# Performance work log

Measured on AMD Instinct MI355X. Metric: run time of the kernel, lower is better.

Reference implementation:

```python
import jax, jax.numpy as jnp
import numpy as np

M, K, N = 131072, 1024, 512


def setup_inputs() -> dict:
    key = jax.random.key(0)
    k1, k2, k3, k4, k5 = jax.random.split(key, 5)
    scale = 0.02
    return {
        "x": jax.random.normal(k1, (M, K), dtype=jnp.float32),
        "w0": jax.random.uniform(k2, (K,), dtype=jnp.float32, minval=0.9, maxval=1.1),
        "w1": jax.random.normal(k3, (K, N), dtype=jnp.float32) * scale,
        "w2": jax.random.normal(k4, (K, N), dtype=jnp.float32) * scale,
        "w3": jax.random.normal(k5, (N, K), dtype=jnp.float32) * scale,
    }


def reference(x, w0, w1, w2, w3):
    # RMSNorm (no eps, matching the kernel): l = rsqrt(mean(x^2))
    l = jax.lax.rsqrt(jnp.sum(x * x, axis=-1) / K)          # [M]
    x1 = x * l[:, None] * w0[None, :]                        # [M, K]
    x2 = x1 @ w1                                             # gate   [M, N]
    y2 = x1 @ w2                                             # up     [M, N]
    x3 = jax.nn.silu(x2) * y2                                # SiLU-gate [M, N]
    out = x3 @ w3                                            # down   [M, K] (skip_connection=False)
    return out
```

## Files before the change

kernel.cpp:

```cpp
#include <hip/hip_runtime.h>
#include <cstdint>

typedef __attribute__((ext_vector_type(4))) float f32x4;
typedef __attribute__((ext_vector_type(8))) short bf16x8;
typedef __attribute__((ext_vector_type(4))) short bf16x4;

#define DEV static __device__ __forceinline__

DEV unsigned short f2bf(float f) {
    union { float f; unsigned int u; } v; v.f = f;
    unsigned int u = v.u;
    return (unsigned short)((u + 0x7FFFu + ((u >> 16) & 1u)) >> 16);
}

DEV void async_cp16(const void* g, void* l) {
    __builtin_amdgcn_global_load_lds(
        (const __attribute__((address_space(1))) unsigned int*)g,
        (__attribute__((address_space(3))) unsigned int*)l,
        16, 0, 0);
}

DEV void stage_half(const unsigned short* __restrict__ g, long kofs,
                    unsigned short* l, int tid, int gpitch) {
#pragma unroll
    for (int i = 0; i < 2; ++i) {
        int c = i * 512 + tid;
        int row = c >> 3;
        int ss = (c & 7) ^ (row & 7);
        async_cp16(g + (long)row * gpitch + kofs + ss * 8,
                   l + (i * 512 + (tid & 448)) * 8);
    }
}

template <int NT>
DEV void gemm256(const unsigned short* __restrict__ gA,
                 const unsigned short* __restrict__ gB,
                 const int gpitch, unsigned short* lds,
                 f32x4 (&acc)[8][4], const int tid) {
    const int lane = tid & 63;
    const int wv = tid >> 6;
    const int wr = wv >> 2;
    const int wcq = wv & 3;
    const int lhi = lane >> 4, llo = lane & 15;
    const int hb = wcq >> 1;
    const int br0 = (wcq & 1) * 64;

#define MFMA8(AF, BF, RI0, CJ0)                                               \
    _Pragma("unroll") for (int kq = 0; kq < 2; ++kq)                          \
    _Pragma("unroll") for (int i = 0; i < 4; ++i)                             \
    _Pragma("unroll") for (int j = 0; j < 2; ++j)                             \
        acc[RI0 + i][CJ0 + j] = __builtin_amdgcn_mfma_f32_16x16x32_bf16(      \
            AF[kq][i], BF[kq][j], acc[RI0 + i][CJ0 + j], 0, 0, 0);

    stage_half(gA, 0, lds + 0 * 8192, tid, gpitch);
    stage_half(gA + (long)128 * gpitch, 0, lds + 1 * 8192, tid, gpitch);
    stage_half(gB, 0, lds + 32768 + 0 * 8192, tid, gpitch);
    stage_half(gB + (long)128 * gpitch, 0, lds + 32768 + 1 * 8192, tid, gpitch);
    if (NT > 1) {
        stage_half(gA, 64, lds + 2 * 8192, tid, gpitch);
        asm volatile("s_waitcnt vmcnt(2)" ::: "memory");
    } else {
        asm volatile("s_waitcnt vmcnt(0)" ::: "memory");
    }
    __builtin_amdgcn_s_barrier();

    bf16x8 af[2][4], bf0[2][2], bf1[2][2];

    for (int kt = 0; kt < NT; ++kt) {
        const int cur = kt & 1, nxt = cur ^ 1;
        const unsigned short* lA = lds + (cur * 2 + wr) * 8192;
        const unsigned short* lB = lds + 32768 + (cur * 2 + hb) * 8192;
        const bool pf1 = (kt + 1 < NT);
        const bool pf2 = (kt + 2 < NT);
        const long k1 = (long)(kt + 1) * 64;
        const long k2 = (long)(kt + 2) * 64;

#pragma unroll
        for (int kq = 0; kq < 2; ++kq) {
            const int q = kq * 4 + lhi;
#pragma unroll
            for (int i = 0; i < 4; ++i) {
                int r = i * 16 + llo;
                af[kq][i] = *(const bf16x8*)&lA[r * 64 + ((q ^ (r & 7)) << 3)];
            }
#pragma unroll
            for (int j = 0; j < 2; ++j) {
                int r = br0 + j * 16 + llo;
                bf0[kq][j] = *(const bf16x8*)&lB[r * 64 + ((q ^ (r & 7)) << 3)];
            }
        }
        if (pf1)
            stage_half(gA + (long)128 * gpitch, k1, lds + (nxt * 2 + 1) * 8192, tid, gpitch);
        __builtin_amdgcn_s_barrier();
        asm volatile("s_waitcnt lgkmcnt(0)");
        __builtin_amdgcn_sched_barrier(0);
        __builtin_amdgcn_s_setprio(1);
        MFMA8(af, bf0, 0, 0)
        __builtin_amdgcn_s_setprio(0);
        __builtin_amdgcn_s_barrier();

#pragma unroll
        for (int kq = 0; kq < 2; ++kq) {
            const int q = kq * 4 + lhi;
#pragma unroll
            for (int j = 0; j < 2; ++j) {
                int r = br0 + 32 + j * 16 + llo;
                bf1[kq][j] = *(const bf16x8*)&lB[r * 64 + ((q ^ (r & 7)) << 3)];
            }
        }
        if (pf1) {
            stage_half(gB, k1, lds + 32768 + (nxt * 2 + 0) * 8192, tid, gpitch);
            stage_half(gB + (long)128 * gpitch, k1, lds + 32768 + (nxt * 2 + 1) * 8192, tid, gpitch);
        }
        __builtin_amdgcn_s_barrier();
        asm volatile("s_waitcnt lgkmcnt(0)");
        __builtin_amdgcn_sched_barrier(0);
        __builtin_amdgcn_s_setprio(1);
        MFMA8(af, bf1, 0, 2)
        __builtin_amdgcn_s_setprio(0);
        __builtin_amdgcn_s_barrier();

#pragma unroll
        for (int kq = 0; kq < 2; ++kq) {
            const int q = kq * 4 + lhi;
#pragma unroll
            for (int i = 0; i < 4; ++i) {
                int r = 64 + i * 16 + llo;
                af[kq][i] = *(const bf16x8*)&lA[r * 64 + ((q ^ (r & 7)) << 3)];
            }
        }
        __builtin_amdgcn_s_barrier();
        asm volatile("s_waitcnt lgkmcnt(0)");
        __builtin_amdgcn_sched_barrier(0);
        __builtin_amdgcn_s_setprio(1);
        MFMA8(af, bf0, 4, 0)
        __builtin_amdgcn_s_setprio(0);
        __builtin_amdgcn_s_barrier();

        if (pf2)
            stage_half(gA, k2, lds + (cur * 2 + 0) * 8192, tid, gpitch);
        __builtin_amdgcn_s_setprio(1);
        MFMA8(af, bf1, 4, 2)
        __builtin_amdgcn_s_setprio(0);
        if (pf1) {
            if (pf2) asm volatile("s_waitcnt vmcnt(2)" ::: "memory");
            else     asm volatile("s_waitcnt vmcnt(0)" ::: "memory");
        }
        __builtin_amdgcn_s_barrier();
        __builtin_amdgcn_sched_barrier(0);
    }
#undef MFMA8
}

__global__ void prep_w(const float* __restrict__ w0, const float* __restrict__ w1,
                       const float* __restrict__ w2, const float* __restrict__ w3,
                       unsigned short* __restrict__ w12t, unsigned short* __restrict__ w3t) {
    int t = blockIdx.x * 256 + threadIdx.x;
    if (t < 1048576) {
        int n = t >> 10, k = t & 1023;
        const float* src = (n & 1) ? w2 : w1;
        w12t[t] = f2bf(w0[k] * src[k * 512 + (n >> 1)]);
    } else {
        int idx = t - 1048576;
        int j = idx >> 9, n = idx & 511;
        w3t[idx] = f2bf(w3[n * 1024 + j]);
    }
}

__global__ __launch_bounds__(256)
void prep_x(const float* __restrict__ x, unsigned short* __restrict__ xb) {
    const int wv = threadIdx.x >> 6, lane = threadIdx.x & 63;
    const int stride = gridDim.x * 4;
    for (int row = blockIdx.x * 4 + wv; row < 131072; row += stride) {
        const float* xr = x + (long)row * 1024;
        f32x4 v[4];
        float s = 0.f;
#pragma unroll
        for (int c = 0; c < 4; ++c) {
            v[c] = *(const f32x4*)(xr + c * 256 + lane * 4);
            s += v[c].x * v[c].x + v[c].y * v[c].y + v[c].z * v[c].z + v[c].w * v[c].w;
        }
#pragma unroll
        for (int off = 32; off > 0; off >>= 1) s += __shfl_xor(s, off, 64);
        float l = rsqrtf(s * (1.0f / 1024.0f));
        unsigned short* xo = xb + (long)row * 1024;
#pragma unroll
        for (int c = 0; c < 4; ++c) {
            bf16x4 b;
            b.x = (short)f2bf(v[c].x * l);
            b.y = (short)f2bf(v[c].y * l);
            b.z = (short)f2bf(v[c].z * l);
            b.w = (short)f2bf(v[c].w * l);
            *(bf16x4*)(xo + c * 256 + lane * 4) = b;
        }
    }
}

__global__ __launch_bounds__(512, 2)
void gate_gemm(const unsigned short* __restrict__ xb,
               const unsigned short* __restrict__ w12t,
               unsigned short* __restrict__ x3) {
    __shared__ unsigned short lds[65536];
    const int tid = threadIdx.x;
    const int lane = tid & 63;
    const int wv = tid >> 6;
    const int wr = wv >> 2, wcq = wv & 3;
    const int lhi = lane >> 4, llo = lane & 15;

    int bid = blockIdx.x;
    int wgid = (bid & 7) * 256 + (bid >> 3);
    const int mt = wgid >> 2, nt = wgid & 3;

    f32x4 acc[8][4];
#pragma unroll
    for (int i = 0; i < 8; ++i)
#pragma unroll
        for (int j = 0; j < 4; ++j) acc[i][j] = (f32x4){0.f, 0.f, 0.f, 0.f};

    gemm256<16>(xb + (long)mt * 256 * 1024, w12t + (long)nt * 256 * 1024,
                1024, lds, acc, tid);

#pragma unroll
    for (int ri = 0; ri < 8; ++ri)
#pragma unroll
        for (int rr = 0; rr < 4; ++rr) {
            int R = wr * 128 + ri * 16 + lhi * 4 + rr;
#pragma unroll
            for (int cj = 0; cj < 4; ++cj) {
                float v = acc[ri][cj][rr];
                float p = __shfl_xor(v, 1, 64);
                float g = (lane & 1) ? p : v;
                float u = (lane & 1) ? v : p;
                float s = (g / (1.0f + __expf(-g))) * u;
                if (!(lane & 1))
                    lds[R * 136 + wcq * 32 + cj * 8 + (llo >> 1)] = f2bf(s);
            }
        }
    __syncthreads();
    unsigned short* xg = x3 + (long)(mt * 256) * 512 + nt * 128;
#pragma unroll
    for (int i = 0; i < 8; ++i) {
        int c = i * 512 + tid;
        int row = c >> 4, ch = c & 15;
        *(bf16x8*)(xg + (long)row * 512 + ch * 8) = *(const bf16x8*)&lds[row * 136 + ch * 8];
    }
}

__global__ __launch_bounds__(512, 2)
void down_gemm(const unsigned short* __restrict__ x3,
               const unsigned short* __restrict__ w3t,
               float* __restrict__ out) {
    __shared__ unsigned short lds[65536];
    const int tid = threadIdx.x;
    const int lane = tid & 63;
    const int wv = tid >> 6;
    const int wr = wv >> 2, wcq = wv & 3;
    const int lhi = lane >> 4, llo = lane & 15;

    int bid = blockIdx.x;
    int wgid = (bid & 7) * 256 + (bid >> 3);
    const int mt = wgid >> 2, nt = wgid & 3;

    f32x4 acc[8][4];
#pragma unroll
    for (int i = 0; i < 8; ++i)
#pragma unroll
        for (int j = 0; j < 4; ++j) acc[i][j] = (f32x4){0.f, 0.f, 0.f, 0.f};

    gemm256<8>(x3 + (long)mt * 256 * 512, w3t + (long)nt * 256 * 512,
               512, lds, acc, tid);

    float* op = out + (long)(mt * 256) * 1024 + nt * 256;
#pragma unroll
    for (int ri = 0; ri < 8; ++ri)
#pragma unroll
        for (int rr = 0; rr < 4; ++rr) {
            int R = wr * 128 + ri * 16 + lhi * 4 + rr;
#pragma unroll
            for (int cj = 0; cj < 4; ++cj)
                op[(long)R * 1024 + wcq * 64 + cj * 16 + llo] = acc[ri][cj][rr];
        }
}

extern "C" void kernel_launch(void* const* d_in, const int* in_sizes, int n_in,
                              void* d_out, int out_size, void* d_ws, size_t ws_size,
                              hipStream_t stream) {
    const float* x  = (const float*)d_in[0];
    const float* w0 = (const float*)d_in[1];
    const float* w1 = (const float*)d_in[2];
    const float* w2 = (const float*)d_in[3];
    const float* w3 = (const float*)d_in[4];
    float* out = (float*)d_out;

    unsigned short* w12t = (unsigned short*)d_ws;
    unsigned short* w3t  = w12t + 1024 * 1024;
    unsigned short* x3   = w3t + 1024 * 512;
    unsigned short* xb   = x3 + (size_t)131072 * 512;

    prep_w<<<dim3(6144), dim3(256), 0, stream>>>(w0, w1, w2, w3, w12t, w3t);
    prep_x<<<dim3(2048), dim3(256), 0, stream>>>(x, xb);
    gate_gemm<<<dim3(2048), dim3(512), 0, stream>>>(xb, w12t, x3);
    down_gemm<<<dim3(2048), dim3(512), 0, stream>>>(x3, w3t, out);
}
```

Baseline: 704.9 us.

## Restructure GEMM main loop to one barrier per K-step with LDS-read prefetch

Rewrites the per-K-tile schedule of the 256x256 bf16 MFMA GEMM. The old loop used several workgroup barriers per tile with lgkmcnt waits before each MFMA group. The new loop drops to a single barrier per K-step and relies on compiler-inserted LDS waits. It also prefetches the next tile's first A/B fragments from LDS during the last MFMA group, using an extra af1 register array. This aims to cut barrier stalls and overlap LDS reads with MFMAs, at the cost of higher register pressure and a stricter vmcnt(0) wait, which may expose global-load latency.

```diff
diff --git a/kernel.cpp b/kernel.cpp
--- a/kernel.cpp
+++ b/kernel.cpp
@@ -30,6 +30,10 @@
         async_cp16(g + (long)row * gpitch + kofs + ss * 8,
                    l + (i * 512 + (tid & 448)) * 8);
     }
+}
+
+DEV bf16x8 ldsrd(const unsigned short* base, int r, int q) {
+    return *(const bf16x8*)&base[r * 64 + ((q ^ (r & 7)) << 3)];
 }
 
 template <int NT>
@@ -45,12 +49,11 @@
     const int hb = wcq >> 1;
     const int br0 = (wcq & 1) * 64;
 
-#define MFMA8(AF, BF, RI0, CJ0)                                               \
-    _Pragma("unroll") for (int kq = 0; kq < 2; ++kq)                          \
+#define MG(AF, BF, KQ, RI0, CJ0)                                              \
     _Pragma("unroll") for (int i = 0; i < 4; ++i)                             \
     _Pragma("unroll") for (int j = 0; j < 2; ++j)                             \
         acc[RI0 + i][CJ0 + j] = __builtin_amdgcn_mfma_f32_16x16x32_bf16(      \
-            AF[kq][i], BF[kq][j], acc[RI0 + i][CJ0 + j], 0, 0, 0);
+            AF[KQ][i], BF[KQ][j], acc[RI0 + i][CJ0 + j], 0, 0, 0);
 
     stage_half(gA, 0, lds + 0 * 8192, tid, gpitch);
     stage_half(gA + (long)128 * gpitch, 0, lds + 1 * 8192, tid, gpitch);
@@ -63,93 +66,80 @@
         asm volatile("s_waitcnt vmcnt(0)" ::: "memory");
     }
     __builtin_amdgcn_s_barrier();
-
-    bf16x8 af[2][4], bf0[2][2], bf1[2][2];
+    __builtin_amdgcn_sched_barrier(0);
+
+    bf16x8 af0[2][4], af1[2][4], bf0[2][2], bf1[2][2];
+
+    {
+        const unsigned short* lA = lds + wr * 8192;
+        const unsigned short* lB = lds + 32768 + hb * 8192;
+#pragma unroll
+        for (int i = 0; i < 4; ++i) af0[0][i] = ldsrd(lA, i * 16 + llo, lhi);
+#pragma unroll
+        for (int j = 0; j < 2; ++j) bf0[0][j] = ldsrd(lB, br0 + j * 16 + llo, lhi);
+    }
 
     for (int kt = 0; kt < NT; ++kt) {
         const int cur = kt & 1, nxt = cur ^ 1;
-        const unsigned short* lA = lds + (cur * 2 + wr) * 8192;
-        const unsigned short* lB = lds + 32768 + (cur * 2 + hb) * 8192;
+        const unsigned short* lA  = lds + (cur * 2 + wr) * 8192;
+        const unsigned short* lB  = lds + 32768 + (cur * 2 + hb) * 8192;
+        const unsigned short* lAn = lds + (nxt * 2 + wr) * 8192;
+        const unsigned short* lBn = lds + 32768 + (nxt * 2 + hb) * 8192;
         const bool pf1 = (kt + 1 < NT);
         const bool pf2 = (kt + 2 < NT);
         const long k1 = (long)(kt + 1) * 64;
         const long k2 = (long)(kt + 2) * 64;
 
 #pragma unroll
-        for (int kq = 0; kq < 2; ++kq) {
-            const int q = kq * 4 + lhi;
-#pragma unroll
-            for (int i = 0; i < 4; ++i) {
-                int r = i * 16 + llo;
-                af[kq][i] = *(const bf16x8*)&lA[r * 64 + ((q ^ (r & 7)) << 3)];
-            }
-#pragma unroll
-            for (int j = 0; j < 2; ++j) {
-                int r = br0 + j * 16 + llo;
-                bf0[kq][j] = *(const bf16x8*)&lB[r * 64 + ((q ^ (r & 7)) << 3)];
-            }
-        }
-        if (pf1)
+        for (int i = 0; i < 4; ++i) af0[1][i] = ldsrd(lA, i * 16 + llo, 4 + lhi);
+#pragma unroll
+        for (int j = 0; j < 2; ++j) bf0[1][j] = ldsrd(lB, br0 + j * 16 + llo, 4 + lhi);
+#pragma unroll
+        for (int kq = 0; kq < 2; ++kq)
+#pragma unroll
+            for (int j = 0; j < 2; ++j)
+                bf1[kq][j] = ldsrd(lB, br0 + 32 + j * 16 + llo, kq * 4 + lhi);
+        if (pf1) {
             stage_half(gA + (long)128 * gpitch, k1, lds + (nxt * 2 + 1) * 8192, tid, gpitch);
-        __builtin_amdgcn_s_barrier();
-        asm volatile("s_waitcnt lgkmcnt(0)");
-        __builtin_amdgcn_sched_barrier(0);
-        __builtin_amdgcn_s_setprio(1);
-        MFMA8(af, bf0, 0, 0)
-        __builtin_amdgcn_s_setprio(0);
-        __builtin_amdgcn_s_barrier();
-
-#pragma unroll
-        for (int kq = 0; kq < 2; ++kq) {
-            const int q = kq * 4 + lhi;
-#pragma unroll
-            for (int j = 0; j < 2; ++j) {
-                int r = br0 + 32 + j * 16 + llo;
-                bf1[kq][j] = *(const bf16x8*)&lB[r * 64 + ((q ^ (r & 7)) << 3)];
-            }
-        }
-        if (pf1) {
             stage_half(gB, k1, lds + 32768 + (nxt * 2 + 0) * 8192, tid, gpitch);
             stage_half(gB + (long)128 * gpitch, k1, lds + 32768 + (nxt * 2 + 1) * 8192, tid, gpitch);
         }
-        __builtin_amdgcn_s_barrier();
-        asm volatile("s_waitcnt lgkmcnt(0)");
-        __builtin_amdgcn_sched_barrier(0);
-        __builtin_amdgcn_s_setprio(1);
-        MFMA8(af, bf1, 0, 2)
-        __builtin_amdgcn_s_setprio(0);
-        __builtin_amdgcn_s_barrier();
-
-#pragma unroll
-        for (int kq = 0; kq < 2; ++kq) {
-            const int q = kq * 4 + lhi;
-#pragma unroll
-            for (int i = 0; i < 4; ++i) {
-                int r = 64 + i * 16 + llo;
-                af[kq][i] = *(const bf16x8*)&lA[r * 64 + ((q ^ (r & 7)) << 3)];
-            }
-        }
-        __builtin_amdgcn_s_barrier();
-        asm volatile("s_waitcnt lgkmcnt(0)");
-        __builtin_amdgcn_sched_barrier(0);
-        __builtin_amdgcn_s_setprio(1);
-        MFMA8(af, bf0, 4, 0)
-        __builtin_amdgcn_s_setprio(0);
-        __builtin_amdgcn_s_barrier();
-
-        if (pf2)
-            stage_half(gA, k2, lds + (cur * 2 + 0) * 8192, tid, gpitch);
-        __builtin_amdgcn_s_setprio(1);
-        MFMA8(af, bf1, 4, 2)
-        __builtin_amdgcn_s_setprio(0);
-        if (pf1) {
-            if (pf2) asm volatile("s_waitcnt vmcnt(2)" ::: "memory");
-            else     asm volatile("s_waitcnt vmcnt(0)" ::: "memory");
-        }
+        __builtin_amdgcn_s_setprio(1);
+        MG(af0, bf0, 0, 0, 0)
+        MG(af0, bf0, 1, 0, 0)
+        __builtin_amdgcn_s_setprio(0);
+
+        __builtin_amdgcn_s_setprio(1);
+        MG(af0, bf1, 0, 0, 2)
+        MG(af0, bf1, 1, 0, 2)
+        __builtin_amdgcn_s_setprio(0);
+
+#pragma unroll
+        for (int kq = 0; kq < 2; ++kq)
+#pragma unroll
+            for (int i = 0; i < 4; ++i)
+                af1[kq][i] = ldsrd(lA, 64 + i * 16 + llo, kq * 4 + lhi);
+        __builtin_amdgcn_s_setprio(1);
+        MG(af1, bf0, 0, 4, 0)
+        MG(af1, bf0, 1, 4, 0)
+        __builtin_amdgcn_s_setprio(0);
+        asm volatile("s_waitcnt vmcnt(0)" ::: "memory");
         __builtin_amdgcn_s_barrier();
         __builtin_amdgcn_sched_barrier(0);
-    }
-#undef MFMA8
+
+        if (pf1) {
+#pragma unroll
+            for (int i = 0; i < 4; ++i) af0[0][i] = ldsrd(lAn, i * 16 + llo, lhi);
+#pragma unroll
+            for (int j = 0; j < 2; ++j) bf0[0][j] = ldsrd(lBn, br0 + j * 16 + llo, lhi);
+        }
+        if (pf2) stage_half(gA, k2, lds + (cur * 2 + 0) * 8192, tid, gpitch);
+        __builtin_amdgcn_s_setprio(1);
+        MG(af1, bf1, 0, 4, 2)
+        MG(af1, bf1, 1, 4, 2)
+        __builtin_amdgcn_s_setprio(0);
+    }
+#undef MG
 }
 
 __global__ void prep_w(const float* __restrict__ w0, const float* __restrict__ w1,
```

New measurement: 710.4 us. About the same (+0.8%).
